# Performance work log

Hardware: AMD Instinct MI355X
Metric: run time of the kernel (lower is better)

## Reference

```python
import jax, jax.numpy as jnp
import numpy as np

EPS = 1e-12

def _l2norm(x):
    # normalize rows so dot product == cosine similarity
    return x / jnp.maximum(jnp.linalg.norm(x, axis=-1, keepdims=True), EPS)

def setup_inputs() -> dict:
    key = jax.random.key(0)
    k1, k2 = jax.random.split(key)
    source_feats = jax.random.normal(k1, (4096, 1024), dtype=jnp.float32)
    target_feats = jax.random.normal(k2, (65536, 1024), dtype=jnp.float32)
    return {"source_feats": source_feats, "target_feats": target_feats, "k": 4}

def reference(source_feats, target_feats, k):
    # cosine kNN matching: for each source frame, find k nearest target frames
    # by cosine distance, then average the (raw) target features.
    sn = _l2norm(source_feats)           # [N, d]
    tn = _l2norm(target_feats)           # [M, d]
    sim = sn @ tn.T                      # [N, M] cosine similarity (dist = 1 - sim)
    _, idx = jax.lax.top_k(sim, k)       # [N, k] highest similarity == smallest cosine distance
    neighbors = target_feats[idx]        # [N, k, d] gather
    out = neighbors.mean(axis=1)         # [N, d]
    return out
```

## Files before the change

kernel.cpp:

```cpp
#include <hip/hip_runtime.h>
#include <math.h>
#include <stdint.h>

#define M     4096
#define NTGT  65536
#define KD    1024

#define NS    32
#define SLICE (NTGT / NS)
#define BT    128
#define BS    256
#define NTILE (SLICE / BT)
#define TSTEP 16
#define TOTST (NTILE * TSTEP)
#define NCAND 256
#define RESC  16
#define BUFSZ 24576

typedef __attribute__((ext_vector_type(4)))  int i32x4;
typedef __attribute__((ext_vector_type(16))) int i32x16;

__device__ __forceinline__ char f2i8(float x) {
    int t = __float2int_rn(x);
    t = t > 127 ? 127 : (t < -127 ? -127 : t);
    return (char)t;
}

template <int NK>
__device__ __forceinline__ void insert_desc_u(uint32_t (&arr)[NK], uint32_t pk) {
    uint32_t cur = pk;
#pragma unroll
    for (int s = 0; s < NK; ++s) {
        uint32_t old = arr[s];
        bool g = cur > old;
        arr[s] = g ? cur : old;
        cur    = g ? old : cur;
    }
}

__device__ __forceinline__ void gload16(const void* g, void* l) {
    __builtin_amdgcn_global_load_lds(
        (const __attribute__((address_space(1))) unsigned int*)g,
        (__attribute__((address_space(3))) unsigned int*)l, 16, 0, 0);
}

__global__ void prep_targets(const float* __restrict__ T, float* __restrict__ tinv,
                             char* __restrict__ Tq) {
    const int wave = threadIdx.x >> 6;
    const int lane = threadIdx.x & 63;
    const int row  = blockIdx.x * 4 + wave;
    const float* p = T + (size_t)row * KD;
    float4 v[4];
    float s = 0.f;
#pragma unroll
    for (int j = 0; j < 4; ++j) {
        v[j] = *reinterpret_cast<const float4*>(p + lane * 4 + j * 256);
        s += v[j].x * v[j].x + v[j].y * v[j].y + v[j].z * v[j].z + v[j].w * v[j].w;
    }
#pragma unroll
    for (int off = 32; off; off >>= 1) s += __shfl_xor(s, off);
    const float rinv = 1.0f / sqrtf(fmaxf(s, 1e-24f));
    if (lane == 0) tinv[row] = rinv;
    const float sc = rinv * 1024.0f;
#pragma unroll
    for (int j = 0; j < 4; ++j) {
        char4 o;
        o.x = f2i8(v[j].x * sc); o.y = f2i8(v[j].y * sc);
        o.z = f2i8(v[j].z * sc); o.w = f2i8(v[j].w * sc);
        *reinterpret_cast<char4*>(Tq + (size_t)row * KD + lane * 4 + j * 256) = o;
    }
}

__global__ void prep_source(const float* __restrict__ S, char* __restrict__ Sq) {
    const int wave = threadIdx.x >> 6;
    const int lane = threadIdx.x & 63;
    const int row  = blockIdx.x * 4 + wave;
    const float* p = S + (size_t)row * KD;
#pragma unroll
    for (int j = 0; j < 4; ++j) {
        float4 v = *reinterpret_cast<const float4*>(p + lane * 4 + j * 256);
        char4 o;
        o.x = f2i8(v.x * 32.0f); o.y = f2i8(v.y * 32.0f);
        o.z = f2i8(v.z * 32.0f); o.w = f2i8(v.w * 32.0f);
        *reinterpret_cast<char4*>(Sq + (size_t)row * KD + lane * 4 + j * 256) = o;
    }
}

__global__ __launch_bounds__(256, 2)
void screen_kernel(const char* __restrict__ Sq, const char* __restrict__ Tq,
                   uint32_t* __restrict__ cand_out) {
    __shared__ __align__(16) unsigned char lds[2 * BUFSZ];

    const int tid  = threadIdx.x;
    const int lane = tid & 63, wc = tid >> 6;
    const int l31 = lane & 31, l5 = lane >> 5;
    const int bx = blockIdx.x;
    const int by = blockIdx.y;
    const int sb   = bx * BS;
    const int tgt0 = by * SLICE;

    const int srow = tid >> 2;
    const int scol = ((tid & 3) ^ ((tid >> 3) & 3)) * 16;
    const char* aStage = Tq + (size_t)(tgt0 + srow) * KD + scol;
    const char* bStage = Sq + (size_t)(sb   + srow) * KD + scol;

    const int s3 = (l31 >> 1) & 3;
    int aOff0[4], aOff1[4], bOff0[2], bOff1[2];
#pragma unroll
    for (int m = 0; m < 4; ++m) {
        const int base = (m * 32 + l31) * 64;
        aOff0[m] = base + ((l5    ) ^ s3) * 16;
        aOff1[m] = base + ((2 + l5) ^ s3) * 16;
    }
#pragma unroll
    for (int nt = 0; nt < 2; ++nt) {
        const int base = 8192 + (wc * 64 + nt * 32 + l31) * 64;
        bOff0[nt] = base + ((l5    ) ^ s3) * 16;
        bOff1[nt] = base + ((2 + l5) ^ s3) * 16;
    }

#define BARX()  __builtin_amdgcn_s_barrier()
#define FENCE() asm volatile("" ::: "memory")
#define VM6()   asm volatile("s_waitcnt vmcnt(6)" ::: "memory")
#define VM0()   asm volatile("s_waitcnt vmcnt(0)" ::: "memory")

#define STAGE(s_) do {                                                         \
        const int tt_ = (s_) >> 4, ks_ = (s_) & 15;                            \
        unsigned char* d_ = lds + (((s_) & 1) ? BUFSZ : 0) + tid * 16;         \
        const char* a_ = aStage + (size_t)(tt_ * BT) * KD + ks_ * 64;          \
        const char* b_ = bStage + ks_ * 64;                                    \
        gload16(a_,            d_);                                            \
        gload16(a_ + 64 * KD,  d_ + 4096);                                     \
        gload16(b_,            d_ + 8192);                                     \
        gload16(b_ + 64 * KD,  d_ + 8192 + 4096);                              \
        gload16(b_ + 128 * KD, d_ + 8192 + 8192);                              \
        gload16(b_ + 192 * KD, d_ + 8192 + 12288);                             \
    } while (0)

    uint32_t cand[2][8];
#pragma unroll
    for (int nt = 0; nt < 2; ++nt)
#pragma unroll
        for (int j = 0; j < 8; ++j) cand[nt][j] = 0u;

    STAGE(0);

#pragma unroll 1
    for (int tt = 0; tt < NTILE; ++tt) {
        i32x16 acc[4][2];
#pragma unroll
        for (int m = 0; m < 4; ++m)
#pragma unroll
            for (int nt = 0; nt < 2; ++nt)
                acc[m][nt] = (i32x16){0,0,0,0, 0,0,0,0, 0,0,0,0, 0,0,0,0};

#pragma unroll 1
        for (int ks = 0; ks < TSTEP; ++ks) {
            const int s = tt * TSTEP + ks;
            if (s + 1 < TOTST) { STAGE(s + 1); VM6(); }
            else               { VM0(); }
            BARX(); FENCE();

            const unsigned char* cb = lds + ((s & 1) ? BUFSZ : 0);
            i32x4 a0[4], a1[4], b0[2], b1[2];
#pragma unroll
            for (int m = 0; m < 4; ++m) {
                a0[m] = *reinterpret_cast<const i32x4*>(cb + aOff0[m]);
                a1[m] = *reinterpret_cast<const i32x4*>(cb + aOff1[m]);
            }
#pragma unroll
            for (int nt = 0; nt < 2; ++nt) {
                b0[nt] = *reinterpret_cast<const i32x4*>(cb + bOff0[nt]);
                b1[nt] = *reinterpret_cast<const i32x4*>(cb + bOff1[nt]);
            }
#pragma unroll
            for (int m = 0; m < 4; ++m)
#pragma unroll
                for (int nt = 0; nt < 2; ++nt) {
                    acc[m][nt] = __builtin_amdgcn_mfma_i32_32x32x32_i8(a0[m], b0[nt], acc[m][nt], 0, 0, 0);
                    acc[m][nt] = __builtin_amdgcn_mfma_i32_32x32x32_i8(a1[m], b1[nt], acc[m][nt], 0, 0, 0);
                }

            FENCE(); BARX();
        }

        const int tb = tgt0 + tt * BT;
#pragma unroll
        for (int nt = 0; nt < 2; ++nt) {
            uint32_t c7 = cand[nt][7];
#pragma unroll
            for (int m = 0; m < 4; ++m) {
#pragma unroll
                for (int r = 0; r < 16; ++r) {
                    const int sc = acc[m][nt][r];
                    int k = (sc + (1 << 20)) >> 5;
                    k = k < 0 ? 0 : (k > 65535 ? 65535 : k);
                    const int tg = tb + m * 32 + (r & 3) + 8 * (r >> 2) + 4 * l5;
                    const uint32_t pk = ((uint32_t)k << 16) | (uint32_t)(tg & 0xFFFF);
                    if (pk > c7) {
                        insert_desc_u<8>(cand[nt], pk);
                        c7 = cand[nt][7];
                    }
                }
            }
        }
    }
#undef STAGE

#pragma unroll
    for (int nt = 0; nt < 2; ++nt) {
        uint32_t inc[8];
#pragma unroll
        for (int j = 0; j < 8; ++j)
            inc[j] = (uint32_t)__shfl_down((int)cand[nt][j], 32);
        if (lane < 32) {
#pragma unroll
            for (int j = 0; j < 8; ++j)
                if (inc[j] > cand[nt][7]) insert_desc_u<8>(cand[nt], inc[j]);
        }
    }

    if (lane < 32) {
#pragma unroll
        for (int nt = 0; nt < 2; ++nt) {
            const int src = sb + wc * 64 + nt * 32 + l31;
            uint32_t* dst = cand_out + (size_t)src * NCAND + by * 8;
            *reinterpret_cast<uint4*>(dst)     = make_uint4(cand[nt][0], cand[nt][1], cand[nt][2], cand[nt][3]);
            *reinterpret_cast<uint4*>(dst + 4) = make_uint4(cand[nt][4], cand[nt][5], cand[nt][6], cand[nt][7]);
        }
    }
}

__global__ __launch_bounds__(256)
void final_kernel(const uint32_t* __restrict__ cand_out, const float* __restrict__ S,
                  const float* __restrict__ T, const float* __restrict__ tinv,
                  float* __restrict__ out) {
    __shared__ __align__(16) float srow[KD];
    __shared__ float rv[RESC];
    __shared__ int   ri[RESC];
    __shared__ int   sel[4];

    const int r = blockIdx.x;
    const int tid = threadIdx.x;

    *reinterpret_cast<float4*>(srow + tid * 4) =
        *reinterpret_cast<const float4*>(S + (size_t)r * KD + tid * 4);

    if (tid < 64) {
        const uint4 cv = *reinterpret_cast<const uint4*>(cand_out + (size_t)r * NCAND + tid * 4);
        uint32_t c0 = cv.x, c1 = cv.y, c2 = cv.z, c3 = cv.w;
#pragma unroll 1
        for (int it = 0; it < RESC; ++it) {
            uint32_t m01 = c0 > c1 ? c0 : c1;
            uint32_t m23 = c2 > c3 ? c2 : c3;
            uint32_t m = m01 > m23 ? m01 : m23;
#pragma unroll
            for (int off = 32; off; off >>= 1) {
                const uint32_t o = (uint32_t)__shfl_xor((int)m, off);
                m = m > o ? m : o;
            }
            if (tid == 0) ri[it] = (int)(m & 0xFFFFu);
            if      (c0 == m) c0 = 0u;
            else if (c1 == m) c1 = 0u;
            else if (c2 == m) c2 = 0u;
            else if (c3 == m) c3 = 0u;
        }
    }
    __syncthreads();

    const int lane = tid & 63, wv = tid >> 6;
    for (int c = wv; c < RESC; c += 4) {
        const int idx = ri[c];
        const float* tp = T + (size_t)idx * KD;
        float s = 0.f;
#pragma unroll
        for (int j = 0; j < 4; ++j) {
            const float4 tv = *reinterpret_cast<const float4*>(tp + lane * 4 + j * 256);
            const float4 sv = *reinterpret_cast<const float4*>(srow + lane * 4 + j * 256);
            s += tv.x * sv.x + tv.y * sv.y + tv.z * sv.z + tv.w * sv.w;
        }
#pragma unroll
        for (int off = 32; off; off >>= 1) s += __shfl_xor(s, off);
        if (lane == 0) rv[c] = s * tinv[idx];
    }
    __syncthreads();

    if (tid == 0) {
        float b0 = -INFINITY, b1 = -INFINITY, b2 = -INFINITY, b3 = -INFINITY;
        int s0 = 0, s1 = 0, s2 = 0, s3 = 0;
        for (int c = 0; c < RESC; ++c) {
            const float v = rv[c]; const int id = ri[c];
            if (v > b3) {
                if (v > b0)      { b3=b2;s3=s2; b2=b1;s2=s1; b1=b0;s1=s0; b0=v;s0=id; }
                else if (v > b1) { b3=b2;s3=s2; b2=b1;s2=s1; b1=v;s1=id; }
                else if (v > b2) { b3=b2;s3=s2; b2=v;s2=id; }
                else             { b3=v;s3=id; }
            }
        }
        sel[0]=s0; sel[1]=s1; sel[2]=s2; sel[3]=s3;
    }
    __syncthreads();

    float4 a = make_float4(0.f, 0.f, 0.f, 0.f);
#pragma unroll
    for (int q = 0; q < 4; ++q) {
        const float4 v = *reinterpret_cast<const float4*>(T + (size_t)sel[q] * KD + tid * 4);
        a.x += v.x; a.y += v.y; a.z += v.z; a.w += v.w;
    }
    a.x *= 0.25f; a.y *= 0.25f; a.z *= 0.25f; a.w *= 0.25f;
    *reinterpret_cast<float4*>(out + (size_t)r * KD + tid * 4) = a;
}

#define FNS    32
#define FSLICE (NTGT / FNS)
#define FBM 128
#define FBN 128
#define FBK 16
#define FNTILE (FSLICE / FBN)
#define FLDA 132
#define FLDSS 33

__global__ void tinv_kernel(const float* __restrict__ T, float* __restrict__ tinv) {
    const int wave = threadIdx.x >> 6;
    const int lane = threadIdx.x & 63;
    const int row  = blockIdx.x * 4 + wave;
    const float* p = T + (size_t)row * KD;
    float s = 0.f;
#pragma unroll
    for (int j = 0; j < 4; ++j) {
        float4 v = *reinterpret_cast<const float4*>(p + lane * 4 + j * 256);
        s += v.x * v.x + v.y * v.y + v.z * v.z + v.w * v.w;
    }
#pragma unroll
    for (int off = 32; off; off >>= 1) s += __shfl_xor(s, off);
    if (lane == 0) tinv[row] = 1.0f / sqrtf(fmaxf(s, 1e-24f));
}

__global__ __launch_bounds__(256, 2)
void simtopk_kernel(const float* __restrict__ S, const float* __restrict__ T,
                    const float* __restrict__ tinv,
                    float* __restrict__ pval, int* __restrict__ pidx) {
    __shared__ float smem[2 * FBK * FLDA];
    __shared__ float tinvS[FBN];
    float* As = smem;
    float* Bs = smem + FBK * FLDA;
    float* Ss = smem;

    const int tid = threadIdx.x;
    const int tx = tid & 15, ty = tid >> 4;
    const int rb   = blockIdx.x;
    const int tgt0 = blockIdx.y * FSLICE;
    const size_t abase = (size_t)(rb * FBM) * KD;

    float t0 = -INFINITY, t1 = -INFINITY, t2 = -INFINITY, t3 = -INFINITY;
    int   i0 = 0, i1 = 0, i2 = 0, i3 = 0;

    for (int nt = 0; nt < FNTILE; ++nt) {
        const int tb = tgt0 + nt * FBN;
        float acc[8][8];
#pragma unroll
        for (int i = 0; i < 8; ++i)
#pragma unroll
            for (int j = 0; j < 8; ++j) acc[i][j] = 0.f;

        for (int kk = 0; kk < KD; kk += FBK) {
            const int rr = tid >> 2;
            const int c4 = (tid & 3) * 4;
#pragma unroll
            for (int h = 0; h < 2; ++h) {
                const int row = rr + h * 64;
                float4 av = *reinterpret_cast<const float4*>(S + abase + (size_t)row * KD + kk + c4);
                float4 bv = *reinterpret_cast<const float4*>(T + (size_t)(tb + row) * KD + kk + c4);
                As[(c4 + 0) * FLDA + row] = av.x; As[(c4 + 1) * FLDA + row] = av.y;
                As[(c4 + 2) * FLDA + row] = av.z; As[(c4 + 3) * FLDA + row] = av.w;
                Bs[(c4 + 0) * FLDA + row] = bv.x; Bs[(c4 + 1) * FLDA + row] = bv.y;
                Bs[(c4 + 2) * FLDA + row] = bv.z; Bs[(c4 + 3) * FLDA + row] = bv.w;
            }
            __syncthreads();
#pragma unroll
            for (int k = 0; k < FBK; ++k) {
                float a[8], b[8];
                *reinterpret_cast<float4*>(&a[0]) = *reinterpret_cast<float4*>(&As[k * FLDA + ty * 8]);
                *reinterpret_cast<float4*>(&a[4]) = *reinterpret_cast<float4*>(&As[k * FLDA + ty * 8 + 4]);
                *reinterpret_cast<float4*>(&b[0]) = *reinterpret_cast<float4*>(&Bs[k * FLDA + tx * 4]);
                *reinterpret_cast<float4*>(&b[4]) = *reinterpret_cast<float4*>(&Bs[k * FLDA + 64 + tx * 4]);
#pragma unroll
                for (int i = 0; i < 8; ++i)
#pragma unroll
                    for (int j = 0; j < 8; ++j)
                        acc[i][j] = fmaf(a[i], b[j], acc[i][j]);
            }
            __syncthreads();
        }

        if (tid < FBN) tinvS[tid] = tinv[tb + tid];
        __syncthreads();

#pragma unroll
        for (int cc = 0; cc < 4; ++cc) {
            const int g = cc >> 1;
            if ((tx >> 3) == (cc & 1)) {
                const int txl = tx & 7;
#pragma unroll
                for (int i = 0; i < 8; ++i) {
                    const int rrow = ty * 8 + i;
#pragma unroll
                    for (int j = 0; j < 4; ++j) {
                        const int colc = 4 * txl + j;
                        Ss[rrow * FLDSS + colc] = acc[i][g * 4 + j] * tinvS[cc * 32 + colc];
                    }
                }
            }
            __syncthreads();
            if (tid < FBM) {
#pragma unroll 4
                for (int c = 0; c < 32; ++c) {
                    const float v = Ss[tid * FLDSS + c];
                    if (v > t3) {
                        const int gi = tb + cc * 32 + c;
                        if (v > t0)      { t3=t2;i3=i2; t2=t1;i2=i1; t1=t0;i1=i0; t0=v;i0=gi; }
                        else if (v > t1) { t3=t2;i3=i2; t2=t1;i2=i1; t1=v;i1=gi; }
                        else if (v > t2) { t3=t2;i3=i2; t2=v;i2=gi; }
                        else             { t3=v;i3=gi; }
                    }
                }
            }
            __syncthreads();
        }
    }

    if (tid < FBM) {
        const int row = rb * FBM + tid;
        const size_t base = ((size_t)blockIdx.y * M + row) * 4;
        pval[base + 0] = t0; pval[base + 1] = t1; pval[base + 2] = t2; pval[base + 3] = t3;
        pidx[base + 0] = i0; pidx[base + 1] = i1; pidx[base + 2] = i2; pidx[base + 3] = i3;
    }
}

__global__ void merge_kernel(const float* __restrict__ pval, const int* __restrict__ pidx,
                             const float* __restrict__ T, float* __restrict__ out) {
    __shared__ float cv[FNS * 4];
    __shared__ int   ci[FNS * 4];
    __shared__ int   sel[4];
    const int r = blockIdx.x;
    const int tid = threadIdx.x;

    if (tid < FNS * 4) {
        const int s = tid >> 2, q = tid & 3;
        const size_t base = ((size_t)s * M + r) * 4 + q;
        cv[tid] = pval[base];
        ci[tid] = pidx[base];
    }
    __syncthreads();

    if (tid == 0) {
        float t0 = -INFINITY, t1 = -INFINITY, t2 = -INFINITY, t3 = -INFINITY;
        int   j0 = 0, j1 = 0, j2 = 0, j3 = 0;
        for (int c = 0; c < FNS * 4; ++c) {
            const float v = cv[c];
            if (v > t3) {
                const int gi = ci[c];
                if (v > t0)      { t3=t2;j3=j2; t2=t1;j2=j1; t1=t0;j1=j0; t0=v;j0=gi; }
                else if (v > t1) { t3=t2;j3=j2; t2=t1;j2=j1; t1=v;j1=gi; }
                else if (v > t2) { t3=t2;j3=j2; t2=v;j2=gi; }
                else             { t3=v;j3=gi; }
            }
        }
        sel[0] = j0; sel[1] = j1; sel[2] = j2; sel[3] = j3;
    }
    __syncthreads();

    const int d = tid * 4;
    float4 a = make_float4(0.f, 0.f, 0.f, 0.f);
#pragma unroll
    for (int q = 0; q < 4; ++q) {
        const float4 v = *reinterpret_cast<const float4*>(T + (size_t)sel[q] * KD + d);
        a.x += v.x; a.y += v.y; a.z += v.z; a.w += v.w;
    }
    a.x *= 0.25f; a.y *= 0.25f; a.z *= 0.25f; a.w *= 0.25f;
    *reinterpret_cast<float4*>(out + (size_t)r * KD + d) = a;
}

extern "C" void kernel_launch(void* const* d_in, const int* in_sizes, int n_in,
                              void* d_out, int out_size, void* d_ws, size_t ws_size,
                              hipStream_t stream) {
    const float* S = (const float*)d_in[0];
    const float* T = (const float*)d_in[1];
    float* out = (float*)d_out;

    const size_t sz_tinv = (size_t)NTGT * 4;
    const size_t sz_Sq   = (size_t)M * KD;
    const size_t sz_Tq   = (size_t)NTGT * KD;
    const size_t sz_cand = (size_t)M * NCAND * 4;
    const size_t need = sz_tinv + sz_Sq + sz_Tq + sz_cand;

    if (ws_size >= need) {
        float*    tinv = (float*)d_ws;
        char*     Sq   = (char*)d_ws + sz_tinv;
        char*     Tq   = (char*)d_ws + sz_tinv + sz_Sq;
        uint32_t* cand = (uint32_t*)((char*)d_ws + sz_tinv + sz_Sq + sz_Tq);

        prep_targets<<<NTGT / 4, 256, 0, stream>>>(T, tinv, Tq);
        prep_source<<<M / 4, 256, 0, stream>>>(S, Sq);
        screen_kernel<<<dim3(M / BS, NS), 256, 0, stream>>>(Sq, Tq, cand);
        final_kernel<<<M, 256, 0, stream>>>(cand, S, T, tinv, out);
    } else {
        float* tinv = (float*)d_ws;
        float* pval = tinv + NTGT;
        int*   pidx = (int*)(pval + (size_t)FNS * M * 4);

        tinv_kernel<<<NTGT / 4, 256, 0, stream>>>(T, tinv);
        simtopk_kernel<<<dim3(M / FBM, FNS), 256, 0, stream>>>(S, T, tinv, pval, pidx);
        merge_kernel<<<M, 256, 0, stream>>>(pval, pidx, T, out);
    }
}
```

Baseline: 475.5 us.

## Prepack int8 operands into MFMA fragment layout and load directly to registers

The prep kernels now store quantized source and target rows in a layout that matches the MFMA 32x32x32 i8 operand fragments. The screen kernel drops its LDS double buffer, swizzling and barriers and instead loads fragments from global memory into two register sets, alternating between them. This is meant to remove LDS traffic and barrier stalls. In exchange, every wave reloads the shared target tile from cache, which multiplies global/L2 traffic and exposes memory latency to the MFMA loop.

```diff
diff --git a/kernel.cpp b/kernel.cpp
--- a/kernel.cpp
+++ b/kernel.cpp
@@ -11,11 +11,10 @@
 #define BT    128
 #define BS    256
 #define NTILE (SLICE / BT)
-#define TSTEP 16
-#define TOTST (NTILE * TSTEP)
+#define KC    32
+#define TOT   (NTILE * KC)
 #define NCAND 256
 #define RESC  16
-#define BUFSZ 24576
 
 typedef __attribute__((ext_vector_type(4)))  int i32x4;
 typedef __attribute__((ext_vector_type(16))) int i32x16;
@@ -38,23 +37,17 @@
     }
 }
 
-__device__ __forceinline__ void gload16(const void* g, void* l) {
-    __builtin_amdgcn_global_load_lds(
-        (const __attribute__((address_space(1))) unsigned int*)g,
-        (__attribute__((address_space(3))) unsigned int*)l, 16, 0, 0);
-}
-
 __global__ void prep_targets(const float* __restrict__ T, float* __restrict__ tinv,
-                             char* __restrict__ Tq) {
+                             char* __restrict__ TqF) {
     const int wave = threadIdx.x >> 6;
     const int lane = threadIdx.x & 63;
     const int row  = blockIdx.x * 4 + wave;
-    const float* p = T + (size_t)row * KD;
+    const float* p = T + (size_t)row * KD + lane * 16;
     float4 v[4];
     float s = 0.f;
 #pragma unroll
     for (int j = 0; j < 4; ++j) {
-        v[j] = *reinterpret_cast<const float4*>(p + lane * 4 + j * 256);
+        v[j] = *reinterpret_cast<const float4*>(p + j * 4);
         s += v[j].x * v[j].x + v[j].y * v[j].y + v[j].z * v[j].z + v[j].w * v[j].w;
     }
 #pragma unroll
@@ -62,35 +55,41 @@
     const float rinv = 1.0f / sqrtf(fmaxf(s, 1e-24f));
     if (lane == 0) tinv[row] = rinv;
     const float sc = rinv * 1024.0f;
+    unsigned char ob[16];
 #pragma unroll
     for (int j = 0; j < 4; ++j) {
-        char4 o;
-        o.x = f2i8(v[j].x * sc); o.y = f2i8(v[j].y * sc);
-        o.z = f2i8(v[j].z * sc); o.w = f2i8(v[j].w * sc);
-        *reinterpret_cast<char4*>(Tq + (size_t)row * KD + lane * 4 + j * 256) = o;
-    }
-}
-
-__global__ void prep_source(const float* __restrict__ S, char* __restrict__ Sq) {
+        ob[j * 4 + 0] = (unsigned char)f2i8(v[j].x * sc);
+        ob[j * 4 + 1] = (unsigned char)f2i8(v[j].y * sc);
+        ob[j * 4 + 2] = (unsigned char)f2i8(v[j].z * sc);
+        ob[j * 4 + 3] = (unsigned char)f2i8(v[j].w * sc);
+    }
+    const int g = row >> 5, kc = lane >> 1, h = lane & 1;
+    char* dst = TqF + (size_t)g * 32768 + (size_t)(kc * 64 + (row & 31) + 32 * h) * 16;
+    *reinterpret_cast<uint4*>(dst) = *reinterpret_cast<const uint4*>(ob);
+}
+
+__global__ void prep_source(const float* __restrict__ S, char* __restrict__ SqF) {
     const int wave = threadIdx.x >> 6;
     const int lane = threadIdx.x & 63;
     const int row  = blockIdx.x * 4 + wave;
-    const float* p = S + (size_t)row * KD;
+    const float* p = S + (size_t)row * KD + lane * 16;
+    unsigned char ob[16];
 #pragma unroll
     for (int j = 0; j < 4; ++j) {
-        float4 v = *reinterpret_cast<const float4*>(p + lane * 4 + j * 256);
-        char4 o;
-        o.x = f2i8(v.x * 32.0f); o.y = f2i8(v.y * 32.0f);
-        o.z = f2i8(v.z * 32.0f); o.w = f2i8(v.w * 32.0f);
-        *reinterpret_cast<char4*>(Sq + (size_t)row * KD + lane * 4 + j * 256) = o;
-    }
+        const float4 v = *reinterpret_cast<const float4*>(p + j * 4);
+        ob[j * 4 + 0] = (unsigned char)f2i8(v.x * 32.0f);
+        ob[j * 4 + 1] = (unsigned char)f2i8(v.y * 32.0f);
+        ob[j * 4 + 2] = (unsigned char)f2i8(v.z * 32.0f);
+        ob[j * 4 + 3] = (unsigned char)f2i8(v.w * 32.0f);
+    }
+    const int g = row >> 5, kc = lane >> 1, h = lane & 1;
+    char* dst = SqF + (size_t)g * 32768 + (size_t)(kc * 64 + (row & 31) + 32 * h) * 16;
+    *reinterpret_cast<uint4*>(dst) = *reinterpret_cast<const uint4*>(ob);
 }
 
 __global__ __launch_bounds__(256, 2)
-void screen_kernel(const char* __restrict__ Sq, const char* __restrict__ Tq,
+void screen_kernel(const char* __restrict__ SqF, const char* __restrict__ TqF,
                    uint32_t* __restrict__ cand_out) {
-    __shared__ __align__(16) unsigned char lds[2 * BUFSZ];
-
     const int tid  = threadIdx.x;
     const int lane = tid & 63, wc = tid >> 6;
     const int l31 = lane & 31, l5 = lane >> 5;
@@ -99,51 +98,38 @@
     const int sb   = bx * BS;
     const int tgt0 = by * SLICE;
 
-    const int srow = tid >> 2;
-    const int scol = ((tid & 3) ^ ((tid >> 3) & 3)) * 16;
-    const char* aStage = Tq + (size_t)(tgt0 + srow) * KD + scol;
-    const char* bStage = Sq + (size_t)(sb   + srow) * KD + scol;
-
-    const int s3 = (l31 >> 1) & 3;
-    int aOff0[4], aOff1[4], bOff0[2], bOff1[2];
-#pragma unroll
-    for (int m = 0; m < 4; ++m) {
-        const int base = (m * 32 + l31) * 64;
-        aOff0[m] = base + ((l5    ) ^ s3) * 16;
-        aOff1[m] = base + ((2 + l5) ^ s3) * 16;
-    }
-#pragma unroll
-    for (int nt = 0; nt < 2; ++nt) {
-        const int base = 8192 + (wc * 64 + nt * 32 + l31) * 64;
-        bOff0[nt] = base + ((l5    ) ^ s3) * 16;
-        bOff1[nt] = base + ((2 + l5) ^ s3) * 16;
-    }
-
-#define BARX()  __builtin_amdgcn_s_barrier()
-#define FENCE() asm volatile("" ::: "memory")
-#define VM6()   asm volatile("s_waitcnt vmcnt(6)" ::: "memory")
-#define VM0()   asm volatile("s_waitcnt vmcnt(0)" ::: "memory")
-
-#define STAGE(s_) do {                                                         \
-        const int tt_ = (s_) >> 4, ks_ = (s_) & 15;                            \
-        unsigned char* d_ = lds + (((s_) & 1) ? BUFSZ : 0) + tid * 16;         \
-        const char* a_ = aStage + (size_t)(tt_ * BT) * KD + ks_ * 64;          \
-        const char* b_ = bStage + ks_ * 64;                                    \
-        gload16(a_,            d_);                                            \
-        gload16(a_ + 64 * KD,  d_ + 4096);                                     \
-        gload16(b_,            d_ + 8192);                                     \
-        gload16(b_ + 64 * KD,  d_ + 8192 + 4096);                              \
-        gload16(b_ + 128 * KD, d_ + 8192 + 8192);                              \
-        gload16(b_ + 192 * KD, d_ + 8192 + 12288);                             \
+    const char* pa = TqF + (size_t)(tgt0 >> 5) * 32768 + lane * 16;
+    const char* pb = SqF + (size_t)((sb >> 5) + wc * 2) * 32768 + lane * 16;
+
+#define LOADF(A, B, gs_) do {                                                  \
+        const int tt_ = (gs_) >> 5, kc_ = (gs_) & 31;                          \
+        const size_t ao_ = (size_t)tt_ * 131072 + (size_t)kc_ * 1024;          \
+        const size_t bo_ = (size_t)kc_ * 1024;                                 \
+        A[0] = *reinterpret_cast<const i32x4*>(pa + ao_);                      \
+        A[1] = *reinterpret_cast<const i32x4*>(pa + ao_ + 32768);              \
+        A[2] = *reinterpret_cast<const i32x4*>(pa + ao_ + 65536);              \
+        A[3] = *reinterpret_cast<const i32x4*>(pa + ao_ + 98304);              \
+        B[0] = *reinterpret_cast<const i32x4*>(pb + bo_);                      \
+        B[1] = *reinterpret_cast<const i32x4*>(pb + bo_ + 32768);              \
     } while (0)
 
+#define MFMA8(A, B) do {                                                       \
+        _Pragma("unroll")                                                      \
+        for (int m = 0; m < 4; ++m)                                            \
+            _Pragma("unroll")                                                  \
+            for (int nt = 0; nt < 2; ++nt)                                     \
+                acc[m][nt] = __builtin_amdgcn_mfma_i32_32x32x32_i8(            \
+                    A[m], B[nt], acc[m][nt], 0, 0, 0);                         \
+    } while (0)
+
     uint32_t cand[2][8];
 #pragma unroll
     for (int nt = 0; nt < 2; ++nt)
 #pragma unroll
         for (int j = 0; j < 8; ++j) cand[nt][j] = 0u;
 
-    STAGE(0);
+    i32x4 aE[4], bE[2], aO[4], bO[2];
+    LOADF(aE, bE, 0);
 
 #pragma unroll 1
     for (int tt = 0; tt < NTILE; ++tt) {
@@ -155,33 +141,12 @@
                 acc[m][nt] = (i32x16){0,0,0,0, 0,0,0,0, 0,0,0,0, 0,0,0,0};
 
 #pragma unroll 1
-        for (int ks = 0; ks < TSTEP; ++ks) {
-            const int s = tt * TSTEP + ks;
-            if (s + 1 < TOTST) { STAGE(s + 1); VM6(); }
-            else               { VM0(); }
-            BARX(); FENCE();
-
-            const unsigned char* cb = lds + ((s & 1) ? BUFSZ : 0);
-            i32x4 a0[4], a1[4], b0[2], b1[2];
-#pragma unroll
-            for (int m = 0; m < 4; ++m) {
-                a0[m] = *reinterpret_cast<const i32x4*>(cb + aOff0[m]);
-                a1[m] = *reinterpret_cast<const i32x4*>(cb + aOff1[m]);
-            }
-#pragma unroll
-            for (int nt = 0; nt < 2; ++nt) {
-                b0[nt] = *reinterpret_cast<const i32x4*>(cb + bOff0[nt]);
-                b1[nt] = *reinterpret_cast<const i32x4*>(cb + bOff1[nt]);
-            }
-#pragma unroll
-            for (int m = 0; m < 4; ++m)
-#pragma unroll
-                for (int nt = 0; nt < 2; ++nt) {
-                    acc[m][nt] = __builtin_amdgcn_mfma_i32_32x32x32_i8(a0[m], b0[nt], acc[m][nt], 0, 0, 0);
-                    acc[m][nt] = __builtin_amdgcn_mfma_i32_32x32x32_i8(a1[m], b1[nt], acc[m][nt], 0, 0, 0);
-                }
-
-            FENCE(); BARX();
+        for (int kcp = 0; kcp < KC / 2; ++kcp) {
+            const int gs = tt * KC + kcp * 2;
+            LOADF(aO, bO, gs + 1);
+            MFMA8(aE, bE);
+            if (gs + 2 < TOT) LOADF(aE, bE, gs + 2);
+            MFMA8(aO, bO);
         }
 
         const int tb = tgt0 + tt * BT;
@@ -205,7 +170,8 @@
             }
         }
     }
-#undef STAGE
+#undef LOADF
+#undef MFMA8
 
 #pragma unroll
     for (int nt = 0; nt < 2; ++nt) {
@@ -496,13 +462,13 @@
 
     if (ws_size >= need) {
         float*    tinv = (float*)d_ws;
-        char*     Sq   = (char*)d_ws + sz_tinv;
-        char*     Tq   = (char*)d_ws + sz_tinv + sz_Sq;
+        char*     SqF  = (char*)d_ws + sz_tinv;
+        char*     TqF  = (char*)d_ws + sz_tinv + sz_Sq;
         uint32_t* cand = (uint32_t*)((char*)d_ws + sz_tinv + sz_Sq + sz_Tq);
 
-        prep_targets<<<NTGT / 4, 256, 0, stream>>>(T, tinv, Tq);
-        prep_source<<<M / 4, 256, 0, stream>>>(S, Sq);
-        screen_kernel<<<dim3(M / BS, NS), 256, 0, stream>>>(Sq, Tq, cand);
+        prep_targets<<<NTGT / 4, 256, 0, stream>>>(T, tinv, TqF);
+        prep_source<<<M / 4, 256, 0, stream>>>(S, SqF);
+        screen_kernel<<<dim3(M / BS, NS), 256, 0, stream>>>(SqF, TqF, cand);
         final_kernel<<<M, 256, 0, stream>>>(cand, S, T, tinv, out);
     } else {
         float* tinv = (float*)d_ws;
```

After: 485.2 us. 1.02x slower.
